# Kernel tuning notes

Hardware: AMD Instinct MI355X
Metric: run time of the kernel (lower is better)

The kernel has to match this reference:

```python
import jax, jax.numpy as jnp
import numpy as np

B, S, UNITS = 32, 2048, 512

def setup_inputs() -> dict:
    key = jax.random.key(0)
    ks = jax.random.split(key, 8)
    sc = 1.0 / np.sqrt(UNITS)
    return {
        "s_prev": jax.random.normal(ks[0], (B, UNITS), jnp.float32),
        "hidden_states": jax.random.normal(ks[1], (B, S, UNITS), jnp.float32),
        "W_kernel": jax.random.normal(ks[2], (UNITS, UNITS), jnp.float32) * sc,
        "W_bias": jnp.zeros((UNITS,), jnp.float32),
        "U_kernel": jax.random.normal(ks[3], (UNITS, UNITS), jnp.float32) * sc,
        "U_bias": jnp.zeros((UNITS,), jnp.float32),
        "V_kernel": jax.random.normal(ks[4], (UNITS, 1), jnp.float32) * sc,
        "V_bias": jnp.zeros((1,), jnp.float32),
    }

def reference(s_prev, hidden_states, W_kernel, W_bias, U_kernel, U_bias, V_kernel, V_bias):
    # NOTE: faithful to the source code: U is applied to s_prev, W to hidden_states,
    # and the context is computed as softmax-weights * s_prev (as written, a quirk
    # of the original module), summed over the sequence axis.
    first = s_prev @ U_kernel + U_bias                      # (B, units)
    second = hidden_states @ W_kernel + W_bias              # (B, S, units)
    score = jnp.tanh(first[:, None, :] + second) @ V_kernel + V_bias  # (B, S, 1)
    weights = jax.nn.softmax(score, axis=1)                 # (B, S, 1)
    context = jnp.sum(weights * s_prev[:, None, :], axis=1) # (B, units)
    return context, weights
```

## Files before the change

kernel.cpp:

```cpp
#include <hip/hip_runtime.h>

#define NBATCH 32
#define SEQ    2048
#define NU     512
#define ASTR   36

typedef __attribute__((ext_vector_type(8)))  short bf16x8;
typedef __attribute__((ext_vector_type(16))) float f32x16;

__device__ __forceinline__ short bf16_rne(float f) {
  union { float f; unsigned u; } v; v.f = f;
  unsigned r = v.u + 0x7fffu + ((v.u >> 16) & 1u);
  return (short)(r >> 16);
}

__device__ __forceinline__ unsigned pk2(float lo, float hi) {
  return __builtin_amdgcn_perm(__float_as_uint(hi), __float_as_uint(lo), 0x07060302u);
}

__device__ __forceinline__ float fast_tanh(float x) {
  float ax = __builtin_fabsf(x);
  float t  = __expf(-2.0f * ax);
  float r  = (1.0f - t) / (1.0f + t);
  return x < 0.0f ? -r : r;
}

__global__ __launch_bounds__(256) void prep_all(const float* __restrict__ W,
                                                const float* __restrict__ sp,
                                                const float* __restrict__ U,
                                                const float* __restrict__ Ub,
                                                const float* __restrict__ Wb,
                                                short* __restrict__ WtSw,
                                                float* __restrict__ first) {
  __shared__ float srow[NU];
  if (blockIdx.x < 1024) {
    int idx = blockIdx.x * 256 + threadIdx.x;
    int col = idx >> 9, k = idx & 511;
    int ksrc = k ^ ((col & 3) << 3);
    WtSw[idx] = bf16_rne(W[(size_t)ksrc * NU + col]);
  } else {
    int blk = blockIdx.x - 1024;
    int b = blk >> 1, half = blk & 1, t = threadIdx.x;
    srow[t]       = sp[b * NU + t];
    srow[t + 256] = sp[b * NU + t + 256];
    __syncthreads();
    int col = half * 256 + t;
    float acc = Ub[col] + Wb[col];
    #pragma unroll 8
    for (int k = 0; k < NU; ++k) acc += srow[k] * U[(size_t)k * NU + col];
    first[b * NU + col] = acc;
  }
}

__global__ __launch_bounds__(256, 3) void attn_main(
    const float* __restrict__ h,
    const short* __restrict__ WtSw,
    const float* __restrict__ first,
    const float* __restrict__ V,
    float* __restrict__ s0)
{
  __shared__ short Alds[2][128 * ASTR];
  __shared__ short Blds[2][128 * 32];
  __shared__ float scores_lds[128];

  const int tid  = threadIdx.x;
  const int lane = tid & 63;
  const int w    = tid >> 6;
  const int wr   = w >> 1, wc = w & 1;
  const int l31  = lane & 31, hi = lane >> 5;

  const int bid = blockIdx.x;
  const int lb  = (bid & 7) * 256 + (bid >> 3);
  const int panel = lb >> 2, q = lb & 3;
  const int rowbase = panel * 128;
  const int b = panel >> 4;

  const int arow  = tid >> 1;
  const int ahalf = tid & 1;
  const float* hA = h + (size_t)(rowbase + arow) * NU + ahalf * 16;
  const int awr   = arow * ASTR + ahalf * 16;

  const short* bsrcB = WtSw + (size_t)(q * 128 + w * 16 + (lane >> 2)) * NU + (lane & 3) * 8;

  #define GLOAD_B(buf, ktn)                                                              \
    {                                                                                    \
      __builtin_amdgcn_global_load_lds(                                                  \
          (const __attribute__((address_space(1))) unsigned*)(bsrcB + (ktn) * 32),       \
          (__attribute__((address_space(3))) unsigned*)(&Blds[buf][w * 512]), 16, 0, 0); \
      __builtin_amdgcn_global_load_lds(                                                  \
          (const __attribute__((address_space(1))) unsigned*)(bsrcB + (ktn) * 32 + 64 * NU), \
          (__attribute__((address_space(3))) unsigned*)(&Blds[buf][2048 + w * 512]), 16, 0, 0); \
      asm volatile("" ::: "memory");                                                     \
    }

  const int rA0 = (wr * 64 + l31) * ASTR + hi * 8;
  const int rA1 = rA0 + 32 * ASTR;
  const int colb0 = wc * 64 + l31;
  const int swb   = colb0 & 3;
  const int bB0 = colb0 * 32, bB1 = bB0 + 32 * 32;

  f32x16 acc[2][2];
  #pragma unroll
  for (int rt = 0; rt < 2; ++rt)
    #pragma unroll
    for (int ct = 0; ct < 2; ++ct)
      #pragma unroll
      for (int r = 0; r < 16; ++r) acc[rt][ct][r] = 0.f;

  float4 ha0, ha1, ha2, ha3;
  float4 hb0, hb1, hb2, hb3;

  #define LOAD_H(V0, V1, V2, V3, ktn)                                       \
    {                                                                       \
      const float* p = hA + (ktn) * 32;                                     \
      V0 = *reinterpret_cast<const float4*>(p + 0);                         \
      V1 = *reinterpret_cast<const float4*>(p + 4);                         \
      V2 = *reinterpret_cast<const float4*>(p + 8);                         \
      V3 = *reinterpret_cast<const float4*>(p + 12);                        \
    }

  #define CVT_WRITE(dst, V0, V1, V2, V3)                                    \
    {                                                                       \
      uint4 u0, u1;                                                         \
      u0.x = pk2(V0.x, V0.y); u0.y = pk2(V0.z, V0.w);                       \
      u0.z = pk2(V1.x, V1.y); u0.w = pk2(V1.z, V1.w);                       \
      u1.x = pk2(V2.x, V2.y); u1.y = pk2(V2.z, V2.w);                       \
      u1.z = pk2(V3.x, V3.y); u1.w = pk2(V3.z, V3.w);                       \
      *reinterpret_cast<uint4*>(&Alds[dst][awr])     = u0;                  \
      *reinterpret_cast<uint4*>(&Alds[dst][awr + 8]) = u1;                  \
    }

  #define COMPUTE(cur)                                                      \
    _Pragma("unroll")                                                       \
    for (int ks = 0; ks < 2; ++ks) {                                        \
      const int sb = ((ks * 2 + hi) ^ swb) << 3;                            \
      bf16x8 af0, af1, bf0, bf1;                                            \
      af0 = *reinterpret_cast<const bf16x8*>(&Alds[cur][rA0 + ks * 16]);    \
      af1 = *reinterpret_cast<const bf16x8*>(&Alds[cur][rA1 + ks * 16]);    \
      bf0 = *reinterpret_cast<const bf16x8*>(&Blds[cur][bB0 + sb]);         \
      bf1 = *reinterpret_cast<const bf16x8*>(&Blds[cur][bB1 + sb]);         \
      acc[0][0] = __builtin_amdgcn_mfma_f32_32x32x16_bf16(af0, bf0, acc[0][0], 0, 0, 0); \
      acc[0][1] = __builtin_amdgcn_mfma_f32_32x32x16_bf16(af0, bf1, acc[0][1], 0, 0, 0); \
      acc[1][0] = __builtin_amdgcn_mfma_f32_32x32x16_bf16(af1, bf0, acc[1][0], 0, 0, 0); \
      acc[1][1] = __builtin_amdgcn_mfma_f32_32x32x16_bf16(af1, bf1, acc[1][1], 0, 0, 0); \
    }

  #define BAR_CNT(N)                                                        \
    asm volatile("s_waitcnt vmcnt(" #N ") lgkmcnt(0)" ::: "memory");        \
    __builtin_amdgcn_s_barrier();                                           \
    asm volatile("" ::: "memory");

  GLOAD_B(0, 0);
  LOAD_H(ha0, ha1, ha2, ha3, 0);
  CVT_WRITE(0, ha0, ha1, ha2, ha3);
  LOAD_H(hb0, hb1, hb2, hb3, 1);
  BAR_CNT(4);

  #pragma unroll 1
  for (int kt2 = 0; kt2 < 6; ++kt2) {
    const int kt = kt2 * 2;
    GLOAD_B(1, kt + 1);
    LOAD_H(ha0, ha1, ha2, ha3, kt + 2);
    COMPUTE(0);
    CVT_WRITE(1, hb0, hb1, hb2, hb3);
    BAR_CNT(4);
    GLOAD_B(0, kt + 2);
    LOAD_H(hb0, hb1, hb2, hb3, kt + 3);
    COMPUTE(1);
    CVT_WRITE(0, ha0, ha1, ha2, ha3);
    BAR_CNT(4);
  }

  GLOAD_B(1, 13);
  LOAD_H(ha0, ha1, ha2, ha3, 14);
  COMPUTE(0);
  CVT_WRITE(1, hb0, hb1, hb2, hb3);
  BAR_CNT(4);

  GLOAD_B(0, 14);
  LOAD_H(hb0, hb1, hb2, hb3, 15);
  COMPUTE(1);
  CVT_WRITE(0, ha0, ha1, ha2, ha3);
  BAR_CNT(4);

  GLOAD_B(1, 15);
  COMPUTE(0);
  CVT_WRITE(1, hb0, hb1, hb2, hb3);
  BAR_CNT(0);

  COMPUTE(1);

  #undef GLOAD_B
  #undef LOAD_H
  #undef CVT_WRITE
  #undef COMPUTE
  #undef BAR_CNT

  float fv[2], vv[2];
  #pragma unroll
  for (int ct = 0; ct < 2; ++ct) {
    int col = q * 128 + wc * 64 + ct * 32 + l31;
    fv[ct] = first[b * NU + col];
    vv[ct] = V[col];
  }
  float part[2][16];
  #pragma unroll
  for (int rt = 0; rt < 2; ++rt) {
    #pragma unroll
    for (int r = 0; r < 16; ++r) {
      float p = 0.f;
      #pragma unroll
      for (int ct = 0; ct < 2; ++ct)
        p += vv[ct] * fast_tanh(fv[ct] + acc[rt][ct][r]);
      #pragma unroll
      for (int m = 1; m < 32; m <<= 1) p += __shfl_xor(p, m, 64);
      part[rt][r] = p;
    }
  }
  __syncthreads();
  if (wc == 0 && l31 == 0) {
    #pragma unroll
    for (int rt = 0; rt < 2; ++rt)
      #pragma unroll
      for (int r = 0; r < 16; ++r)
        scores_lds[wr * 64 + rt * 32 + (r & 3) + 8 * (r >> 2) + 4 * hi] = part[rt][r];
  }
  __syncthreads();
  if (wc == 1 && l31 == 0) {
    #pragma unroll
    for (int rt = 0; rt < 2; ++rt)
      #pragma unroll
      for (int r = 0; r < 16; ++r)
        scores_lds[wr * 64 + rt * 32 + (r & 3) + 8 * (r >> 2) + 4 * hi] += part[rt][r];
  }
  __syncthreads();
  if (tid < 128) atomicAdd(&s0[rowbase + tid], scores_lds[tid]);
}

__global__ __launch_bounds__(256) void softmax_ctx(const float* __restrict__ sp,
                                                   float* __restrict__ out) {
  const int b = blockIdx.x;
  const int t = threadIdx.x;
  float* wgt = out + NBATCH * NU + (size_t)b * SEQ;
  __shared__ float red[4];

  float v[8];
  float mx = -1e30f;
  #pragma unroll
  for (int i = 0; i < 8; ++i) { v[i] = wgt[t + i * 256]; mx = fmaxf(mx, v[i]); }
  #pragma unroll
  for (int m = 1; m < 64; m <<= 1) mx = fmaxf(mx, __shfl_xor(mx, m, 64));
  if ((t & 63) == 0) red[t >> 6] = mx;
  __syncthreads();
  mx = fmaxf(fmaxf(red[0], red[1]), fmaxf(red[2], red[3]));
  __syncthreads();

  float se = 0.f;
  #pragma unroll
  for (int i = 0; i < 8; ++i) { v[i] = __expf(v[i] - mx); se += v[i]; }
  #pragma unroll
  for (int m = 1; m < 64; m <<= 1) se += __shfl_xor(se, m, 64);
  if ((t & 63) == 0) red[t >> 6] = se;
  __syncthreads();
  se = red[0] + red[1] + red[2] + red[3];
  __syncthreads();

  const float inv = 1.0f / se;
  float sw = 0.f;
  #pragma unroll
  for (int i = 0; i < 8; ++i) { float wi = v[i] * inv; wgt[t + i * 256] = wi; sw += wi; }
  #pragma unroll
  for (int m = 1; m < 64; m <<= 1) sw += __shfl_xor(sw, m, 64);
  if ((t & 63) == 0) red[t >> 6] = sw;
  __syncthreads();
  sw = red[0] + red[1] + red[2] + red[3];

  out[b * NU + t]       = sp[b * NU + t] * sw;
  out[b * NU + t + 256] = sp[b * NU + t + 256] * sw;
}

extern "C" void kernel_launch(void* const* d_in, const int* in_sizes, int n_in,
                              void* d_out, int out_size, void* d_ws, size_t ws_size,
                              hipStream_t stream) {
  (void)in_sizes; (void)n_in; (void)out_size; (void)ws_size;
  const float* s_prev = (const float*)d_in[0];
  const float* h      = (const float*)d_in[1];
  const float* Wk     = (const float*)d_in[2];
  const float* Wb     = (const float*)d_in[3];
  const float* Uk     = (const float*)d_in[4];
  const float* Ub     = (const float*)d_in[5];
  const float* Vk     = (const float*)d_in[6];

  float* out   = (float*)d_out;
  float* first = (float*)d_ws;
  short* WtSw  = (short*)((char*)d_ws + 65536);
  float* s0    = out + NBATCH * NU;

  hipMemsetAsync(s0, 0, (size_t)NBATCH * SEQ * sizeof(float), stream);
  prep_all   <<<1088, 256, 0, stream>>>(Wk, s_prev, Uk, Ub, Wb, WtSw, first);
  attn_main  <<<2048, 256, 0, stream>>>(h, WtSw, first, Vk, s0);
  softmax_ctx<<<  32, 256, 0, stream>>>(s_prev, out);
}
```

Before: 117.4 us.

## Enlarge attention GEMM tile to 256 rows and stage W through registers

Each attn_main block now covers 256 sequence rows with 512 threads, so each block reuses its W column tile across twice as many rows and the grid is halved. W is now stored as a plain transposed bf16 matrix. It is loaded with ordinary global loads into registers and written to a padded LDS buffer, replacing the async global_load_lds path and the XOR swizzle. The explicit vmcnt barriers become plain __syncthreads. Requesting launch_bounds(512,4) tightens the per-thread register budget, which risks spilling the 64-float accumulator. The async load overlap is also lost.

New measurement: 110.5 us. 5.9% less time.

```diff
diff --git a/kernel.cpp b/kernel.cpp
--- a/kernel.cpp
+++ b/kernel.cpp
@@ -30,14 +30,13 @@
                                                 const float* __restrict__ U,
                                                 const float* __restrict__ Ub,
                                                 const float* __restrict__ Wb,
-                                                short* __restrict__ WtSw,
+                                                short* __restrict__ Wt,
                                                 float* __restrict__ first) {
   __shared__ float srow[NU];
   if (blockIdx.x < 1024) {
     int idx = blockIdx.x * 256 + threadIdx.x;
-    int col = idx >> 9, k = idx & 511;
-    int ksrc = k ^ ((col & 3) << 3);
-    WtSw[idx] = bf16_rne(W[(size_t)ksrc * NU + col]);
+    int u = idx >> 9, k = idx & 511;
+    Wt[(size_t)u * NU + k] = bf16_rne(W[(size_t)k * NU + u]);
   } else {
     int blk = blockIdx.x - 1024;
     int b = blk >> 1, half = blk & 1, t = threadIdx.x;
@@ -52,16 +51,16 @@
   }
 }
 
-__global__ __launch_bounds__(256, 3) void attn_main(
+__global__ __launch_bounds__(512, 4) void attn_main(
     const float* __restrict__ h,
-    const short* __restrict__ WtSw,
+    const short* __restrict__ Wt,
     const float* __restrict__ first,
     const float* __restrict__ V,
     float* __restrict__ s0)
 {
-  __shared__ short Alds[2][128 * ASTR];
-  __shared__ short Blds[2][128 * 32];
-  __shared__ float scores_lds[128];
+  __shared__ short Alds[2][256 * ASTR];
+  __shared__ short Blds[2][128 * ASTR];
+  __shared__ float scores_lds[256];
 
   const int tid  = threadIdx.x;
   const int lane = tid & 63;
@@ -70,34 +69,22 @@
   const int l31  = lane & 31, hi = lane >> 5;
 
   const int bid = blockIdx.x;
-  const int lb  = (bid & 7) * 256 + (bid >> 3);
+  const int lb  = (bid & 7) * 128 + (bid >> 3);
   const int panel = lb >> 2, q = lb & 3;
-  const int rowbase = panel * 128;
-  const int b = panel >> 4;
+  const int rowbase = panel * 256;
+  const int b = panel >> 3;
 
   const int arow  = tid >> 1;
   const int ahalf = tid & 1;
   const float* hA = h + (size_t)(rowbase + arow) * NU + ahalf * 16;
   const int awr   = arow * ASTR + ahalf * 16;
-
-  const short* bsrcB = WtSw + (size_t)(q * 128 + w * 16 + (lane >> 2)) * NU + (lane & 3) * 8;
-
-  #define GLOAD_B(buf, ktn)                                                              \
-    {                                                                                    \
-      __builtin_amdgcn_global_load_lds(                                                  \
-          (const __attribute__((address_space(1))) unsigned*)(bsrcB + (ktn) * 32),       \
-          (__attribute__((address_space(3))) unsigned*)(&Blds[buf][w * 512]), 16, 0, 0); \
-      __builtin_amdgcn_global_load_lds(                                                  \
-          (const __attribute__((address_space(1))) unsigned*)(bsrcB + (ktn) * 32 + 64 * NU), \
-          (__attribute__((address_space(3))) unsigned*)(&Blds[buf][2048 + w * 512]), 16, 0, 0); \
-      asm volatile("" ::: "memory");                                                     \
-    }
+  const short* bsrc = Wt + (size_t)(q * 128 + (tid >> 2)) * NU + (tid & 3) * 8;
+  const int bwr   = (tid >> 2) * ASTR + (tid & 3) * 8;
 
   const int rA0 = (wr * 64 + l31) * ASTR + hi * 8;
   const int rA1 = rA0 + 32 * ASTR;
-  const int colb0 = wc * 64 + l31;
-  const int swb   = colb0 & 3;
-  const int bB0 = colb0 * 32, bB1 = bB0 + 32 * 32;
+  const int rB0 = (wc * 64 + l31) * ASTR + hi * 8;
+  const int rB1 = rB0 + 32 * ASTR;
 
   f32x16 acc[2][2];
   #pragma unroll
@@ -109,6 +96,7 @@
 
   float4 ha0, ha1, ha2, ha3;
   float4 hb0, hb1, hb2, hb3;
+  int4   bq0;
 
   #define LOAD_H(V0, V1, V2, V3, ktn)                                       \
     {                                                                       \
@@ -128,73 +116,54 @@
       u1.z = pk2(V3.x, V3.y); u1.w = pk2(V3.z, V3.w);                       \
       *reinterpret_cast<uint4*>(&Alds[dst][awr])     = u0;                  \
       *reinterpret_cast<uint4*>(&Alds[dst][awr + 8]) = u1;                  \
+      *reinterpret_cast<int4*>(&Blds[dst][bwr])      = bq0;                 \
     }
 
   #define COMPUTE(cur)                                                      \
     _Pragma("unroll")                                                       \
     for (int ks = 0; ks < 2; ++ks) {                                        \
-      const int sb = ((ks * 2 + hi) ^ swb) << 3;                            \
       bf16x8 af0, af1, bf0, bf1;                                            \
       af0 = *reinterpret_cast<const bf16x8*>(&Alds[cur][rA0 + ks * 16]);    \
       af1 = *reinterpret_cast<const bf16x8*>(&Alds[cur][rA1 + ks * 16]);    \
-      bf0 = *reinterpret_cast<const bf16x8*>(&Blds[cur][bB0 + sb]);         \
-      bf1 = *reinterpret_cast<const bf16x8*>(&Blds[cur][bB1 + sb]);         \
+      bf0 = *reinterpret_cast<const bf16x8*>(&Blds[cur][rB0 + ks * 16]);    \
+      bf1 = *reinterpret_cast<const bf16x8*>(&Blds[cur][rB1 + ks * 16]);    \
       acc[0][0] = __builtin_amdgcn_mfma_f32_32x32x16_bf16(af0, bf0, acc[0][0], 0, 0, 0); \
       acc[0][1] = __builtin_amdgcn_mfma_f32_32x32x16_bf16(af0, bf1, acc[0][1], 0, 0, 0); \
       acc[1][0] = __builtin_amdgcn_mfma_f32_32x32x16_bf16(af1, bf0, acc[1][0], 0, 0, 0); \
       acc[1][1] = __builtin_amdgcn_mfma_f32_32x32x16_bf16(af1, bf1, acc[1][1], 0, 0, 0); \
     }
 
-  #define BAR_CNT(N)                                                        \
-    asm volatile("s_waitcnt vmcnt(" #N ") lgkmcnt(0)" ::: "memory");        \
-    __builtin_amdgcn_s_barrier();                                           \
-    asm volatile("" ::: "memory");
-
-  GLOAD_B(0, 0);
+  bq0 = *reinterpret_cast<const int4*>(bsrc);
   LOAD_H(ha0, ha1, ha2, ha3, 0);
   CVT_WRITE(0, ha0, ha1, ha2, ha3);
   LOAD_H(hb0, hb1, hb2, hb3, 1);
-  BAR_CNT(4);
+  __syncthreads();
 
   #pragma unroll 1
-  for (int kt2 = 0; kt2 < 6; ++kt2) {
+  for (int kt2 = 0; kt2 < 7; ++kt2) {
     const int kt = kt2 * 2;
-    GLOAD_B(1, kt + 1);
+    bq0 = *reinterpret_cast<const int4*>(bsrc + (kt + 1) * 32);
     LOAD_H(ha0, ha1, ha2, ha3, kt + 2);
     COMPUTE(0);
     CVT_WRITE(1, hb0, hb1, hb2, hb3);
-    BAR_CNT(4);
-    GLOAD_B(0, kt + 2);
+    __syncthreads();
+    bq0 = *reinterpret_cast<const int4*>(bsrc + (kt + 2) * 32);
     LOAD_H(hb0, hb1, hb2, hb3, kt + 3);
     COMPUTE(1);
     CVT_WRITE(0, ha0, ha1, ha2, ha3);
-    BAR_CNT(4);
-  }
-
-  GLOAD_B(1, 13);
-  LOAD_H(ha0, ha1, ha2, ha3, 14);
+    __syncthreads();
+  }
+
+  bq0 = *reinterpret_cast<const int4*>(bsrc + 15 * 32);
   COMPUTE(0);
   CVT_WRITE(1, hb0, hb1, hb2, hb3);
-  BAR_CNT(4);
-
-  GLOAD_B(0, 14);
-  LOAD_H(hb0, hb1, hb2, hb3, 15);
+  __syncthreads();
+
   COMPUTE(1);
-  CVT_WRITE(0, ha0, ha1, ha2, ha3);
-  BAR_CNT(4);
-
-  GLOAD_B(1, 15);
-  COMPUTE(0);
-  CVT_WRITE(1, hb0, hb1, hb2, hb3);
-  BAR_CNT(0);
-
-  COMPUTE(1);
-
-  #undef GLOAD_B
+
   #undef LOAD_H
   #undef CVT_WRITE
   #undef COMPUTE
-  #undef BAR_CNT
 
   float fv[2], vv[2];
   #pragma unroll
@@ -234,7 +203,7 @@
         scores_lds[wr * 64 + rt * 32 + (r & 3) + 8 * (r >> 2) + 4 * hi] += part[rt][r];
   }
   __syncthreads();
-  if (tid < 128) atomicAdd(&s0[rowbase + tid], scores_lds[tid]);
+  if (tid < 256) atomicAdd(&s0[rowbase + tid], scores_lds[tid]);
 }
 
 __global__ __launch_bounds__(256) void softmax_ctx(const float* __restrict__ sp,
@@ -293,11 +262,11 @@
 
   float* out   = (float*)d_out;
   float* first = (float*)d_ws;
-  short* WtSw  = (short*)((char*)d_ws + 65536);
+  short* Wt    = (short*)((char*)d_ws + 65536);
   float* s0    = out + NBATCH * NU;
 
   hipMemsetAsync(s0, 0, (size_t)NBATCH * SEQ * sizeof(float), stream);
-  prep_all   <<<1088, 256, 0, stream>>>(Wk, s_prev, Uk, Ub, Wb, WtSw, first);
-  attn_main  <<<2048, 256, 0, stream>>>(h, WtSw, first, Vk, s0);
+  prep_all   <<<1088, 256, 0, stream>>>(Wk, s_prev, Uk, Ub, Wb, Wt, first);
+  attn_main  <<<1024, 512, 0, stream>>>(h, Wt, first, Vk, s0);
   softmax_ctx<<<  32, 256, 0, stream>>>(s_prev, out);
 }
```
